# Kernel optimization log

Measured on AMD Instinct MI355X. Metric: run time of the kernel, lower is better.

The kernel has to match this reference:

```python
import jax, jax.numpy as jnp
import numpy as np

N_NODES = 50000
N_EDGES = 800000
D_HIDDEN = 128
N_LAYERS = 3


def setup_inputs() -> dict:
    key = jax.random.key(0)
    k1, k2, k3 = jax.random.split(key, 3)
    x = jax.random.normal(k1, (N_NODES, D_HIDDEN), dtype=jnp.float32)
    edge_index = jax.random.randint(k2, (2, N_EDGES), 0, N_NODES, dtype=jnp.int32)
    # per-layer GCNConv params: weight [d,d], bias [d] (PyG lin has bias merged into conv bias)
    Ws = jax.random.normal(k3, (N_LAYERS, D_HIDDEN, D_HIDDEN), dtype=jnp.float32) / np.sqrt(D_HIDDEN).astype(np.float32)
    bs = jnp.zeros((N_LAYERS, D_HIDDEN), dtype=jnp.float32)
    return {"x": x, "edge_index": edge_index, "Ws": Ws, "bs": bs}


def reference(x, edge_index, Ws, bs):
    n = x.shape[0]
    # PyG GCNConv default: add self-loops, symmetric degree normalization.
    loops = jnp.arange(n, dtype=edge_index.dtype)
    src = jnp.concatenate([edge_index[0], loops])  # message sources (x_j)
    dst = jnp.concatenate([edge_index[1], loops])  # aggregation targets
    deg = jax.ops.segment_sum(jnp.ones_like(src, dtype=x.dtype), dst, num_segments=n)
    dinv = jnp.where(deg > 0, jax.lax.rsqrt(deg), jnp.zeros_like(deg))
    norm = dinv[src] * dinv[dst]  # [E+N]; edge_index is static across layers so compute once
    for l in range(Ws.shape[0]):
        h = x @ Ws[l]                                  # dense linear [N, d]
        msg = h[src] * norm[:, None]                   # gather + normalize [E+N, d]
        x = jax.ops.segment_sum(msg, dst, num_segments=n) + bs[l]  # scatter-add
    # single GELU applied after the final layer (per the original forward)
    x = jax.nn.gelu(x, approximate=False)
    return x
```

## Files before the change

kernel.cpp:

```cpp
#include <hip/hip_runtime.h>
#include <math.h>

#define D 128

typedef __attribute__((ext_vector_type(8))) short short8v;
typedef __attribute__((ext_vector_type(4))) float f32x4;

__device__ __forceinline__ unsigned short f2bf(float x) {
    unsigned int u = __float_as_uint(x);
    unsigned int r = (u + 0x7FFFu + ((u >> 16) & 1u)) >> 16;
    return (unsigned short)r;
}
__device__ __forceinline__ float bf2f(unsigned short b) {
    return __uint_as_float(((unsigned int)b) << 16);
}


__global__ void prep_k(const float* __restrict__ Wp, short* __restrict__ BFh,
                       short* __restrict__ BFl, int wtot,
                       int* __restrict__ cnt, int N) {
    int idx = blockIdx.x * blockDim.x + threadIdx.x;
    if (idx < wtot) {
        int i    = idx & 7;
        int lane = (idx >> 3) & 63;
        int ct   = (idx >> 9) & 7;
        int ks   = (idx >> 12) & 3;
        int l    = idx >> 14;
        int k = ks * 32 + (lane >> 4) * 8 + i;
        int n = ct * 16 + (lane & 15);
        float w = Wp[(size_t)l * (D * D) + (size_t)k * D + n];
        unsigned short h = f2bf(w);
        BFh[idx] = (short)h;
        BFl[idx] = (short)f2bf(w - bf2f(h));
    }
    if (idx < N) cnt[idx] = 0;
}


__global__ void rank_k(const int* __restrict__ dst, int E,
                       int* __restrict__ cnt, unsigned short* __restrict__ rank) {
    int e = blockIdx.x * blockDim.x + threadIdx.x;
    if (e < E) rank[e] = (unsigned short)atomicAdd(&cnt[dst[e]], 1);
}

__global__ __launch_bounds__(1024) void scan_a(const int* __restrict__ cnt, int N,
                                               int* __restrict__ part, int* __restrict__ bsum) {
    __shared__ int s[1024];
    int i = blockIdx.x * 1024 + threadIdx.x;
    int v = (i < N) ? cnt[i] : 0;
    s[threadIdx.x] = v;
    __syncthreads();
    for (int off = 1; off < 1024; off <<= 1) {
        int add = (threadIdx.x >= off) ? s[threadIdx.x - off] : 0;
        __syncthreads();
        s[threadIdx.x] += add;
        __syncthreads();
    }
    if (i < N) part[i] = s[threadIdx.x] - v;
    if (threadIdx.x == 1023) bsum[blockIdx.x] = s[1023];
}

__global__ __launch_bounds__(256) void scan_c(const int* __restrict__ cnt, int* __restrict__ part,
                                              const int* __restrict__ bsum,
                                              float* __restrict__ dinv, int N, int E) {
    __shared__ int s_pref;
    int chunk = blockIdx.x >> 2;
    if (threadIdx.x < 64) {
        int v = (threadIdx.x < chunk) ? bsum[threadIdx.x] : 0;
#pragma unroll
        for (int off = 1; off < 64; off <<= 1) v += __shfl_xor(v, off);
        if (threadIdx.x == 0) s_pref = v;
    }
    __syncthreads();
    int i = blockIdx.x * blockDim.x + threadIdx.x;
    if (i < N) {
        part[i] = part[i] + s_pref;
        dinv[i] = rsqrtf((float)(cnt[i] + 1));
    }
    if (i == 0) part[N] = E;
}


__device__ __forceinline__ void stage_w(const short* __restrict__ BFh,
                                        const short* __restrict__ BFl,
                                        uint4* __restrict__ WH, uint4* __restrict__ WL,
                                        int tid) {
    const uint4* gh = (const uint4*)BFh;
    const uint4* gl = (const uint4*)BFl;
#pragma unroll
    for (int i = 0; i < 8; ++i) WH[tid + i * 256] = gh[tid + i * 256];
#pragma unroll
    for (int i = 0; i < 8; ++i) WL[tid + i * 256] = gl[tid + i * 256];
}

__device__ __forceinline__ void mfma_phase(short8v ah[4], short8v al[4],
                                           const uint4* __restrict__ WH,
                                           const uint4* __restrict__ WL,
                                           const float* __restrict__ dinv,
                                           unsigned short* __restrict__ Hb, int M,
                                           int rowBase, int lane) {
    int rb = rowBase + (lane >> 4) * 4;
    float dsc[4];
#pragma unroll
    for (int i = 0; i < 4; ++i) dsc[i] = (rb + i < M) ? dinv[rb + i] : 0.f;

    const short8v* Bh = (const short8v*)WH;
    const short8v* Bl = (const short8v*)WL;
#pragma unroll
    for (int ct = 0; ct < 8; ++ct) {
        short8v bh[4], bl[4];
#pragma unroll
        for (int ks = 0; ks < 4; ++ks) {
            bh[ks] = Bh[(ks * 8 + ct) * 64 + lane];
            bl[ks] = Bl[(ks * 8 + ct) * 64 + lane];
        }
        f32x4 acc = {0.f, 0.f, 0.f, 0.f};
#pragma unroll
        for (int ks = 0; ks < 4; ++ks) {
            acc = __builtin_amdgcn_mfma_f32_16x16x32_bf16(ah[ks], bh[ks], acc, 0, 0, 0);
            acc = __builtin_amdgcn_mfma_f32_16x16x32_bf16(al[ks], bh[ks], acc, 0, 0, 0);
            acc = __builtin_amdgcn_mfma_f32_16x16x32_bf16(ah[ks], bl[ks], acc, 0, 0, 0);
        }
        int c = ct * 16 + (lane & 15);
#pragma unroll
        for (int i = 0; i < 4; ++i) {
            int r = rb + i;
            if (r < M) Hb[(size_t)r * D + c] = f2bf(dsc[i] * acc[i]);
        }
    }
}

__device__ __forceinline__ void load_a_f32(const float* __restrict__ X, int M,
                                           int rowBase, int lane,
                                           short8v ah[4], short8v al[4]) {
    int arow = rowBase + (lane & 15);
    bool aval = arow < M;
    const float* xr = X + (size_t)arow * D + (lane >> 4) * 8;
#pragma unroll
    for (int ks = 0; ks < 4; ++ks) {
        float4 p = make_float4(0.f, 0.f, 0.f, 0.f);
        float4 q = make_float4(0.f, 0.f, 0.f, 0.f);
        if (aval) {
            p = *(const float4*)(xr + ks * 32);
            q = *(const float4*)(xr + ks * 32 + 4);
        }
        float v[8] = {p.x, p.y, p.z, p.w, q.x, q.y, q.z, q.w};
#pragma unroll
        for (int i = 0; i < 8; ++i) {
            unsigned short h = f2bf(v[i]);
            ah[ks][i] = (short)h;
            al[ks][i] = (short)f2bf(v[i] - bf2f(h));
        }
    }
}

__global__ __launch_bounds__(256) void gemm2_k(const unsigned short* __restrict__ XH,
                                               const unsigned short* __restrict__ XL,
                                               const short* __restrict__ BFh,
                                               const short* __restrict__ BFl,
                                               const float* __restrict__ dinv,
                                               unsigned short* __restrict__ Hb, int M) {
    __shared__ uint4 WH[2048];
    __shared__ uint4 WL[2048];
    stage_w(BFh, BFl, WH, WL, threadIdx.x);

    int lane = threadIdx.x & 63;
    int rowBase = blockIdx.x * 64 + (threadIdx.x >> 6) * 16;
    int arow = rowBase + (lane & 15);
    bool aval = arow < M;
    const unsigned short* xh = XH + (size_t)arow * D + (lane >> 4) * 8;
    const unsigned short* xl = XL + (size_t)arow * D + (lane >> 4) * 8;

    short8v ah[4], al[4];
#pragma unroll
    for (int ks = 0; ks < 4; ++ks) {
        short8v zh = {0,0,0,0,0,0,0,0};
        short8v zl = {0,0,0,0,0,0,0,0};
        if (aval) {
            zh = *(const short8v*)(xh + ks * 32);
            zl = *(const short8v*)(xl + ks * 32);
        }
        ah[ks] = zh;
        al[ks] = zl;
    }
    __syncthreads();
    mfma_phase(ah, al, WH, WL, dinv, Hb, M, rowBase, lane);
}

__global__ __launch_bounds__(256) void fillgemm_k(const float* __restrict__ X,
                                                  const short* __restrict__ BFh,
                                                  const short* __restrict__ BFl,
                                                  const float* __restrict__ dinv,
                                                  unsigned short* __restrict__ Hb, int M, int gb,
                                                  const int* __restrict__ src,
                                                  const int* __restrict__ dst,
                                                  const unsigned short* __restrict__ rank,
                                                  const int* __restrict__ rp, int E,
                                                  unsigned short* __restrict__ ssrc) {
    __shared__ uint4 WH[2048];
    __shared__ uint4 WL[2048];
    if ((int)blockIdx.x < gb) {
        stage_w(BFh, BFl, WH, WL, threadIdx.x);
        int lane = threadIdx.x & 63;
        int rowBase = blockIdx.x * 64 + (threadIdx.x >> 6) * 16;
        short8v ah[4], al[4];
        load_a_f32(X, M, rowBase, lane, ah, al);
        __syncthreads();
        mfma_phase(ah, al, WH, WL, dinv, Hb, M, rowBase, lane);
    } else {
        int e = (blockIdx.x - gb) * blockDim.x + threadIdx.x;
        if (e < E) {
            int p = rp[dst[e]] + (int)rank[e];
            ssrc[p] = (unsigned short)src[e];
        }
    }
}


__device__ __forceinline__ float gelu_f(float x) {
    return 0.5f * x * (1.0f + erff(x * 0.70710678118654752f));
}

__global__ __launch_bounds__(256) void agg_k(const unsigned short* __restrict__ Hb,
                                             const int* __restrict__ rp,
                                             const unsigned short* __restrict__ ssrc,
                                             const float* __restrict__ dinv,
                                             const float* __restrict__ bias,
                                             float* __restrict__ outF,
                                             unsigned short* __restrict__ outH,
                                             unsigned short* __restrict__ outL,
                                             int N, int mode) {
    int node = blockIdx.x * 4 + (threadIdx.x >> 6);
    int lane = threadIdx.x & 63;
    if (node >= N) return;
    const uint4* __restrict__ hb4 = (const uint4*)Hb;
    int grp = lane >> 4;
    int sub = lane & 15;

    float acc[8];
#pragma unroll
    for (int i = 0; i < 8; ++i) acc[i] = 0.f;

    int e0 = rp[node];
    int e1 = rp[node + 1];
    for (int base = e0; base < e1; base += 64) {
        int idxv = 0;
        if (base + lane < e1) idxv = (int)ssrc[base + lane];
        int cnt = e1 - base; if (cnt > 64) cnt = 64;
        for (int c = 0; c < cnt; c += 16) {
            uint4 v[4];
#pragma unroll
            for (int j = 0; j < 4; ++j) {
                int row = __shfl(idxv, c + 4 * j + grp);
                v[j] = hb4[(size_t)row * 16 + sub];
            }
#pragma unroll
            for (int j = 0; j < 4; ++j) {
                bool ok = (base + c + 4 * j + grp) < e1;
                unsigned int w;
                w = ok ? v[j].x : 0u;
                acc[0] += __uint_as_float(w << 16); acc[1] += __uint_as_float(w & 0xFFFF0000u);
                w = ok ? v[j].y : 0u;
                acc[2] += __uint_as_float(w << 16); acc[3] += __uint_as_float(w & 0xFFFF0000u);
                w = ok ? v[j].z : 0u;
                acc[4] += __uint_as_float(w << 16); acc[5] += __uint_as_float(w & 0xFFFF0000u);
                w = ok ? v[j].w : 0u;
                acc[6] += __uint_as_float(w << 16); acc[7] += __uint_as_float(w & 0xFFFF0000u);
            }
        }
    }
#pragma unroll
    for (int i = 0; i < 8; ++i) {
        acc[i] += __shfl_xor(acc[i], 16);
        acc[i] += __shfl_xor(acc[i], 32);
    }
    if (lane < 16) {
        uint4 sv = hb4[(size_t)node * 16 + lane];
        acc[0] += __uint_as_float(sv.x << 16); acc[1] += __uint_as_float(sv.x & 0xFFFF0000u);
        acc[2] += __uint_as_float(sv.y << 16); acc[3] += __uint_as_float(sv.y & 0xFFFF0000u);
        acc[4] += __uint_as_float(sv.z << 16); acc[5] += __uint_as_float(sv.z & 0xFFFF0000u);
        acc[6] += __uint_as_float(sv.w << 16); acc[7] += __uint_as_float(sv.w & 0xFFFF0000u);
        float dn = dinv[node];
        float4 b0 = ((const float4*)bias)[lane * 2];
        float4 b1 = ((const float4*)bias)[lane * 2 + 1];
        float r[8];
        r[0] = dn * acc[0] + b0.x; r[1] = dn * acc[1] + b0.y;
        r[2] = dn * acc[2] + b0.z; r[3] = dn * acc[3] + b0.w;
        r[4] = dn * acc[4] + b1.x; r[5] = dn * acc[5] + b1.y;
        r[6] = dn * acc[6] + b1.z; r[7] = dn * acc[7] + b1.w;
        if (mode) {
#pragma unroll
            for (int i = 0; i < 8; ++i) r[i] = gelu_f(r[i]);
            float4 o0 = make_float4(r[0], r[1], r[2], r[3]);
            float4 o1 = make_float4(r[4], r[5], r[6], r[7]);
            ((float4*)outF)[(size_t)node * 32 + lane * 2]     = o0;
            ((float4*)outF)[(size_t)node * 32 + lane * 2 + 1] = o1;
        } else {
            unsigned short h[8], lo[8];
#pragma unroll
            for (int i = 0; i < 8; ++i) {
                h[i]  = f2bf(r[i]);
                lo[i] = f2bf(r[i] - bf2f(h[i]));
            }
            uint4 ph, pl;
            ph.x = (unsigned int)h[0]  | ((unsigned int)h[1] << 16);
            ph.y = (unsigned int)h[2]  | ((unsigned int)h[3] << 16);
            ph.z = (unsigned int)h[4]  | ((unsigned int)h[5] << 16);
            ph.w = (unsigned int)h[6]  | ((unsigned int)h[7] << 16);
            pl.x = (unsigned int)lo[0] | ((unsigned int)lo[1] << 16);
            pl.y = (unsigned int)lo[2] | ((unsigned int)lo[3] << 16);
            pl.z = (unsigned int)lo[4] | ((unsigned int)lo[5] << 16);
            pl.w = (unsigned int)lo[6] | ((unsigned int)lo[7] << 16);
            ((uint4*)outH)[(size_t)node * 16 + lane] = ph;
            ((uint4*)outL)[(size_t)node * 16 + lane] = pl;
        }
    }
}


extern "C" void kernel_launch(void* const* d_in, const int* in_sizes, int n_in,
                              void* d_out, int out_size, void* d_ws, size_t ws_size,
                              hipStream_t stream) {
    const float* X  = (const float*)d_in[0];
    const int*   EI = (const int*)d_in[1];
    const float* Wp = (const float*)d_in[2];
    const float* bp = (const float*)d_in[3];
    float* OUT = (float*)d_out;

    int N = in_sizes[0] / D;
    int E = in_sizes[1] / 2;
    int L = in_sizes[3] / D;
    const int* src = EI;
    const int* dst = EI + E;

    char* w = (char*)d_ws;
    auto alloc = [&](size_t bytes) {
        char* p = w;
        w += (bytes + 255) & ~(size_t)255;
        return p;
    };
    unsigned short* HB  = (unsigned short*)alloc((size_t)(N + 64) * D * sizeof(unsigned short));
    unsigned short* XH  = (unsigned short*)alloc((size_t)(N + 64) * D * sizeof(unsigned short));
    unsigned short* XL  = (unsigned short*)alloc((size_t)(N + 64) * D * sizeof(unsigned short));
    float* DINV = (float*)alloc((size_t)N * sizeof(float));
    int*   RP   = (int*)alloc((size_t)(N + 1) * sizeof(int));
    int*   CNT  = (int*)alloc((size_t)N * sizeof(int));
    int*   BSUM = (int*)alloc(4096 * sizeof(int));
    unsigned short* RANK = (unsigned short*)alloc((size_t)E * sizeof(unsigned short));
    unsigned short* SSRC = (unsigned short*)alloc(((size_t)E + 64) * sizeof(unsigned short));
    short* BFH  = (short*)alloc((size_t)L * D * D * sizeof(short));
    short* BFL  = (short*)alloc((size_t)L * D * D * sizeof(short));
    (void)ws_size; (void)n_in; (void)out_size;

    int wtot = L * D * D;
    int pb = ((N > wtot ? N : wtot) + 255) / 256;
    prep_k<<<pb, 256, 0, stream>>>(Wp, BFH, BFL, wtot, CNT, N);

    int eb = (E + 255) / 256;
    rank_k<<<eb, 256, 0, stream>>>(dst, E, CNT, RANK);
    int nb = (N + 1023) / 1024;
    scan_a<<<nb, 1024, 0, stream>>>(CNT, N, RP, BSUM);
    scan_c<<<(N + 255) / 256, 256, 0, stream>>>(CNT, RP, BSUM, DINV, N, E);

    int gb = (N + 63) / 64;
    fillgemm_k<<<gb + eb, 256, 0, stream>>>(X, BFH, BFL, DINV, HB, N, gb,
                                            src, dst, RANK, RP, E, SSRC);

    int ab = (N + 3) / 4;
    agg_k<<<ab, 256, 0, stream>>>(HB, RP, SSRC, DINV, bp, nullptr, XH, XL, N, 0);
    gemm2_k<<<gb, 256, 0, stream>>>(XH, XL, BFH + (size_t)1 * D * D, BFL + (size_t)1 * D * D,
                                    DINV, HB, N);
    agg_k<<<ab, 256, 0, stream>>>(HB, RP, SSRC, DINV, bp + D, nullptr, XH, XL, N, 0);
    gemm2_k<<<gb, 256, 0, stream>>>(XH, XL, BFH + (size_t)2 * D * D, BFL + (size_t)2 * D * D,
                                    DINV, HB, N);
    agg_k<<<ab, 256, 0, stream>>>(HB, RP, SSRC, DINV, bp + 2 * D, OUT, nullptr, nullptr, N, 1);
}
```

Baseline: 201.4 us.

## Merge scan into single-block kernel, drop LDS weight staging in fillgemm

Replaces the two-kernel prefix scan (block scan plus fixup) with one single-block kernel in which each thread scans a contiguous chunk serially, removing a launch and the block-sum buffer. The first-layer GEMM in fillgemm_k now reads weight fragments straight from global memory instead of staging them in LDS, which frees 64KB of shared memory per block so the edge-fill blocks can have higher occupancy. agg_k also issues its self-loop row load before the neighbour loop so that load latency overlaps with the loop. Risks are the serial per-thread scan on a single workgroup, whose chunked cnt accesses are poorly coalesced, and the extra global or cache traffic from repeated weight loads.

```diff
diff --git a/kernel.cpp b/kernel.cpp
--- a/kernel.cpp
+++ b/kernel.cpp
@@ -43,92 +43,39 @@
     if (e < E) rank[e] = (unsigned short)atomicAdd(&cnt[dst[e]], 1);
 }
 
-__global__ __launch_bounds__(1024) void scan_a(const int* __restrict__ cnt, int N,
-                                               int* __restrict__ part, int* __restrict__ bsum) {
+__global__ __launch_bounds__(1024) void scan_k(const int* __restrict__ cnt,
+                                               int* __restrict__ rp,
+                                               float* __restrict__ dinv, int N, int E) {
     __shared__ int s[1024];
-    int i = blockIdx.x * 1024 + threadIdx.x;
-    int v = (i < N) ? cnt[i] : 0;
-    s[threadIdx.x] = v;
+    int t = threadIdx.x;
+    int CH = (N + 1023) >> 10;
+    int i0 = t * CH;
+    int sum = 0;
+    for (int j = 0; j < CH; ++j) {
+        int i = i0 + j;
+        if (i < N) sum += cnt[i];
+    }
+    s[t] = sum;
     __syncthreads();
     for (int off = 1; off < 1024; off <<= 1) {
-        int add = (threadIdx.x >= off) ? s[threadIdx.x - off] : 0;
+        int add = (t >= off) ? s[t - off] : 0;
         __syncthreads();
-        s[threadIdx.x] += add;
+        s[t] += add;
         __syncthreads();
     }
-    if (i < N) part[i] = s[threadIdx.x] - v;
-    if (threadIdx.x == 1023) bsum[blockIdx.x] = s[1023];
-}
-
-__global__ __launch_bounds__(256) void scan_c(const int* __restrict__ cnt, int* __restrict__ part,
-                                              const int* __restrict__ bsum,
-                                              float* __restrict__ dinv, int N, int E) {
-    __shared__ int s_pref;
-    int chunk = blockIdx.x >> 2;
-    if (threadIdx.x < 64) {
-        int v = (threadIdx.x < chunk) ? bsum[threadIdx.x] : 0;
-#pragma unroll
-        for (int off = 1; off < 64; off <<= 1) v += __shfl_xor(v, off);
-        if (threadIdx.x == 0) s_pref = v;
-    }
-    __syncthreads();
-    int i = blockIdx.x * blockDim.x + threadIdx.x;
-    if (i < N) {
-        part[i] = part[i] + s_pref;
-        dinv[i] = rsqrtf((float)(cnt[i] + 1));
-    }
-    if (i == 0) part[N] = E;
-}
-
-
-__device__ __forceinline__ void stage_w(const short* __restrict__ BFh,
-                                        const short* __restrict__ BFl,
-                                        uint4* __restrict__ WH, uint4* __restrict__ WL,
-                                        int tid) {
-    const uint4* gh = (const uint4*)BFh;
-    const uint4* gl = (const uint4*)BFl;
-#pragma unroll
-    for (int i = 0; i < 8; ++i) WH[tid + i * 256] = gh[tid + i * 256];
-#pragma unroll
-    for (int i = 0; i < 8; ++i) WL[tid + i * 256] = gl[tid + i * 256];
-}
-
-__device__ __forceinline__ void mfma_phase(short8v ah[4], short8v al[4],
-                                           const uint4* __restrict__ WH,
-                                           const uint4* __restrict__ WL,
-                                           const float* __restrict__ dinv,
-                                           unsigned short* __restrict__ Hb, int M,
-                                           int rowBase, int lane) {
-    int rb = rowBase + (lane >> 4) * 4;
-    float dsc[4];
-#pragma unroll
-    for (int i = 0; i < 4; ++i) dsc[i] = (rb + i < M) ? dinv[rb + i] : 0.f;
-
-    const short8v* Bh = (const short8v*)WH;
-    const short8v* Bl = (const short8v*)WL;
-#pragma unroll
-    for (int ct = 0; ct < 8; ++ct) {
-        short8v bh[4], bl[4];
-#pragma unroll
-        for (int ks = 0; ks < 4; ++ks) {
-            bh[ks] = Bh[(ks * 8 + ct) * 64 + lane];
-            bl[ks] = Bl[(ks * 8 + ct) * 64 + lane];
-        }
-        f32x4 acc = {0.f, 0.f, 0.f, 0.f};
-#pragma unroll
-        for (int ks = 0; ks < 4; ++ks) {
-            acc = __builtin_amdgcn_mfma_f32_16x16x32_bf16(ah[ks], bh[ks], acc, 0, 0, 0);
-            acc = __builtin_amdgcn_mfma_f32_16x16x32_bf16(al[ks], bh[ks], acc, 0, 0, 0);
-            acc = __builtin_amdgcn_mfma_f32_16x16x32_bf16(ah[ks], bl[ks], acc, 0, 0, 0);
-        }
-        int c = ct * 16 + (lane & 15);
-#pragma unroll
-        for (int i = 0; i < 4; ++i) {
-            int r = rb + i;
-            if (r < M) Hb[(size_t)r * D + c] = f2bf(dsc[i] * acc[i]);
-        }
-    }
-}
+    int pref = s[t] - sum;
+    for (int j = 0; j < CH; ++j) {
+        int i = i0 + j;
+        if (i < N) {
+            int c = cnt[i];
+            rp[i] = pref;
+            pref += c;
+            dinv[i] = rsqrtf((float)(c + 1));
+        }
+    }
+    if (t == 0) rp[N] = E;
+}
+
 
 __device__ __forceinline__ void load_a_f32(const float* __restrict__ X, int M,
                                            int rowBase, int lane,
@@ -150,6 +97,80 @@
             unsigned short h = f2bf(v[i]);
             ah[ks][i] = (short)h;
             al[ks][i] = (short)f2bf(v[i] - bf2f(h));
+        }
+    }
+}
+
+__device__ __forceinline__ void mfma_phase_g(short8v ah[4], short8v al[4],
+                                             const short* __restrict__ BFh,
+                                             const short* __restrict__ BFl,
+                                             const float* __restrict__ dinv,
+                                             unsigned short* __restrict__ Hb, int M,
+                                             int rowBase, int lane) {
+    int rb = rowBase + (lane >> 4) * 4;
+    float dsc[4];
+#pragma unroll
+    for (int i = 0; i < 4; ++i) dsc[i] = (rb + i < M) ? dinv[rb + i] : 0.f;
+
+    const short8v* Bh = (const short8v*)BFh;
+    const short8v* Bl = (const short8v*)BFl;
+#pragma unroll
+    for (int ct = 0; ct < 8; ++ct) {
+        short8v bh[4], bl[4];
+#pragma unroll
+        for (int ks = 0; ks < 4; ++ks) {
+            bh[ks] = Bh[(ks * 8 + ct) * 64 + lane];
+            bl[ks] = Bl[(ks * 8 + ct) * 64 + lane];
+        }
+        f32x4 acc = {0.f, 0.f, 0.f, 0.f};
+#pragma unroll
+        for (int ks = 0; ks < 4; ++ks) {
+            acc = __builtin_amdgcn_mfma_f32_16x16x32_bf16(ah[ks], bh[ks], acc, 0, 0, 0);
+            acc = __builtin_amdgcn_mfma_f32_16x16x32_bf16(al[ks], bh[ks], acc, 0, 0, 0);
+            acc = __builtin_amdgcn_mfma_f32_16x16x32_bf16(ah[ks], bl[ks], acc, 0, 0, 0);
+        }
+        int c = ct * 16 + (lane & 15);
+#pragma unroll
+        for (int i = 0; i < 4; ++i) {
+            int r = rb + i;
+            if (r < M) Hb[(size_t)r * D + c] = f2bf(dsc[i] * acc[i]);
+        }
+    }
+}
+
+__device__ __forceinline__ void mfma_phase_l(short8v ah[4], short8v al[4],
+                                             const uint4* __restrict__ WH,
+                                             const uint4* __restrict__ WL,
+                                             const float* __restrict__ dinv,
+                                             unsigned short* __restrict__ Hb, int M,
+                                             int rowBase, int lane) {
+    int rb = rowBase + (lane >> 4) * 4;
+    float dsc[4];
+#pragma unroll
+    for (int i = 0; i < 4; ++i) dsc[i] = (rb + i < M) ? dinv[rb + i] : 0.f;
+
+    const short8v* Bh = (const short8v*)WH;
+    const short8v* Bl = (const short8v*)WL;
+#pragma unroll
+    for (int ct = 0; ct < 8; ++ct) {
+        short8v bh[4], bl[4];
+#pragma unroll
+        for (int ks = 0; ks < 4; ++ks) {
+            bh[ks] = Bh[(ks * 8 + ct) * 64 + lane];
+            bl[ks] = Bl[(ks * 8 + ct) * 64 + lane];
+        }
+        f32x4 acc = {0.f, 0.f, 0.f, 0.f};
+#pragma unroll
+        for (int ks = 0; ks < 4; ++ks) {
+            acc = __builtin_amdgcn_mfma_f32_16x16x32_bf16(ah[ks], bh[ks], acc, 0, 0, 0);
+            acc = __builtin_amdgcn_mfma_f32_16x16x32_bf16(al[ks], bh[ks], acc, 0, 0, 0);
+            acc = __builtin_amdgcn_mfma_f32_16x16x32_bf16(ah[ks], bl[ks], acc, 0, 0, 0);
+        }
+        int c = ct * 16 + (lane & 15);
+#pragma unroll
+        for (int i = 0; i < 4; ++i) {
+            int r = rb + i;
+            if (r < M) Hb[(size_t)r * D + c] = f2bf(dsc[i] * acc[i]);
         }
     }
 }
@@ -162,7 +183,15 @@
                                                unsigned short* __restrict__ Hb, int M) {
     __shared__ uint4 WH[2048];
     __shared__ uint4 WL[2048];
-    stage_w(BFh, BFl, WH, WL, threadIdx.x);
+    {
+        const uint4* gh = (const uint4*)BFh;
+        const uint4* gl = (const uint4*)BFl;
+        int t = threadIdx.x;
+#pragma unroll
+        for (int i = 0; i < 8; ++i) WH[t + i * 256] = gh[t + i * 256];
+#pragma unroll
+        for (int i = 0; i < 8; ++i) WL[t + i * 256] = gl[t + i * 256];
+    }
 
     int lane = threadIdx.x & 63;
     int rowBase = blockIdx.x * 64 + (threadIdx.x >> 6) * 16;
@@ -184,7 +213,7 @@
         al[ks] = zl;
     }
     __syncthreads();
-    mfma_phase(ah, al, WH, WL, dinv, Hb, M, rowBase, lane);
+    mfma_phase_l(ah, al, WH, WL, dinv, Hb, M, rowBase, lane);
 }
 
 __global__ __launch_bounds__(256) void fillgemm_k(const float* __restrict__ X,
@@ -197,16 +226,12 @@
                                                   const unsigned short* __restrict__ rank,
                                                   const int* __restrict__ rp, int E,
                                                   unsigned short* __restrict__ ssrc) {
-    __shared__ uint4 WH[2048];
-    __shared__ uint4 WL[2048];
     if ((int)blockIdx.x < gb) {
-        stage_w(BFh, BFl, WH, WL, threadIdx.x);
         int lane = threadIdx.x & 63;
         int rowBase = blockIdx.x * 64 + (threadIdx.x >> 6) * 16;
         short8v ah[4], al[4];
         load_a_f32(X, M, rowBase, lane, ah, al);
-        __syncthreads();
-        mfma_phase(ah, al, WH, WL, dinv, Hb, M, rowBase, lane);
+        mfma_phase_g(ah, al, BFh, BFl, dinv, Hb, M, rowBase, lane);
     } else {
         int e = (blockIdx.x - gb) * blockDim.x + threadIdx.x;
         if (e < E) {
@@ -237,6 +262,9 @@
     int grp = lane >> 4;
     int sub = lane & 15;
 
+    uint4 sv = make_uint4(0u, 0u, 0u, 0u);
+    if (lane < 16) sv = hb4[(size_t)node * 16 + lane];
+
     float acc[8];
 #pragma unroll
     for (int i = 0; i < 8; ++i) acc[i] = 0.f;
@@ -275,7 +303,6 @@
         acc[i] += __shfl_xor(acc[i], 32);
     }
     if (lane < 16) {
-        uint4 sv = hb4[(size_t)node * 16 + lane];
         acc[0] += __uint_as_float(sv.x << 16); acc[1] += __uint_as_float(sv.x & 0xFFFF0000u);
         acc[2] += __uint_as_float(sv.y << 16); acc[3] += __uint_as_float(sv.y & 0xFFFF0000u);
         acc[4] += __uint_as_float(sv.z << 16); acc[5] += __uint_as_float(sv.z & 0xFFFF0000u);
@@ -345,7 +372,6 @@
     float* DINV = (float*)alloc((size_t)N * sizeof(float));
     int*   RP   = (int*)alloc((size_t)(N + 1) * sizeof(int));
     int*   CNT  = (int*)alloc((size_t)N * sizeof(int));
-    int*   BSUM = (int*)alloc(4096 * sizeof(int));
     unsigned short* RANK = (unsigned short*)alloc((size_t)E * sizeof(unsigned short));
     unsigned short* SSRC = (unsigned short*)alloc(((size_t)E + 64) * sizeof(unsigned short));
     short* BFH  = (short*)alloc((size_t)L * D * D * sizeof(short));
@@ -358,9 +384,7 @@
 
     int eb = (E + 255) / 256;
     rank_k<<<eb, 256, 0, stream>>>(dst, E, CNT, RANK);
-    int nb = (N + 1023) / 1024;
-    scan_a<<<nb, 1024, 0, stream>>>(CNT, N, RP, BSUM);
-    scan_c<<<(N + 255) / 256, 256, 0, stream>>>(CNT, RP, BSUM, DINV, N, E);
+    scan_k<<<1, 1024, 0, stream>>>(CNT, RP, DINV, N, E);
 
     int gb = (N + 63) / 64;
     fillgemm_k<<<gb + eb, 256, 0, stream>>>(X, BFH, BFL, DINV, HB, N, gb,
```

New measurement: 316.6 us. 57.2% more time.
